# Optimization experiments

Measured on AMD Instinct MI355X. Metric: run time of the kernel, lower is better.

The kernel has to match this reference:

```python
import jax, jax.numpy as jnp
import numpy as np

B, T, F_IN, H = 512, 512, 64, 128
BN_EPS = 1e-3  # Keras BatchNormalization default epsilon


def setup_inputs() -> dict:
    key = jax.random.key(0)
    ks = jax.random.split(key, 12)
    x = jax.random.normal(ks[0], (B, T, F_IN), dtype=jnp.float32)
    # last channel is a discrete phase index in {0,1,2}, stored as float
    state = jax.random.randint(ks[1], (B, T, 1), 0, 3).astype(jnp.float32)
    inputs = jnp.concatenate([x, state], axis=-1)  # [B, T, F_IN+1]
    s = 1.0 / np.sqrt(H)
    return {
        "inputs": inputs,
        "Wx": jax.random.normal(ks[2], (F_IN, 3 * H), dtype=jnp.float32) * s,
        "Wh": jax.random.normal(ks[3], (H, 3 * H), dtype=jnp.float32) * s,
        "b": jax.random.normal(ks[4], (2, 3 * H), dtype=jnp.float32) * 0.01,
        "W_state": jax.random.normal(ks[5], (3, H), dtype=jnp.float32),
        "w1": jax.random.normal(ks[6], (H, 64), dtype=jnp.float32) * s,
        "b1": jnp.zeros((64,), jnp.float32),
        "gamma": jnp.ones((64,), jnp.float32),
        "beta": jnp.zeros((64,), jnp.float32),
        "mean": jnp.zeros((64,), jnp.float32),
        "var": jnp.ones((64,), jnp.float32),
        "w2": jax.random.normal(ks[7], (64, 1), dtype=jnp.float32) * 0.125,
        "b2": jnp.zeros((1,), jnp.float32),
    }


def _gru_final_state(x, Wx, Wh, b):
    # Keras GRU, reset_after=True (default): separate input / recurrent biases.
    b_in, b_rec = b[0], b[1]
    xw = x @ Wx + b_in                      # [B, T, 3H] (precompute input matmuls)
    xw_t = jnp.swapaxes(xw, 0, 1)           # [T, B, 3H]
    h0 = jnp.zeros((x.shape[0], Wh.shape[0]), x.dtype)

    def step(h, xw_step):
        rec = h @ Wh + b_rec                # [B, 3H]
        xz, xr, xh = jnp.split(xw_step, 3, axis=-1)
        rz, rr, rh = jnp.split(rec, 3, axis=-1)
        z = jax.nn.sigmoid(xz + rz)
        r = jax.nn.sigmoid(xr + rr)
        hh = jnp.tanh(xh + r * rh)
        h_new = z * h + (1.0 - z) * hh
        return h_new, None

    h_final, _ = jax.lax.scan(step, h0, xw_t)
    return h_final                          # [B, H]


def reference(inputs, Wx, Wh, b, W_state, w1, b1, gamma, beta, mean, var, w2, b2):
    x = inputs[:, :, :-1]                   # [B, T, F_IN]
    state = inputs[:, :, -1]                # [B, T]
    hidden = _gru_final_state(x, Wx, Wh, b)  # [B, H]
    idx = jnp.clip(state[:, -1].astype(jnp.int32), 0, W_state.shape[0] - 1)
    hidden = hidden + W_state[idx]          # gather-add phase effect
    h = jax.nn.relu(hidden @ w1 + b1)       # dense1
    # dropout: identity in inference mode
    h = (h - mean) * jax.lax.rsqrt(var + BN_EPS) * gamma + beta  # batchnorm (inference)
    return h @ w2 + b2                      # [B, 1]
```

## Files before the change

kernel.cpp:

```cpp
#include <hip/hip_runtime.h>
#include <hip/hip_bf16.h>

#define T_SEQ   512
#define H_DIM   128
#define N3H     384
#define HSW     128
#define XS      72

typedef float f32x4 __attribute__((ext_vector_type(4)));
typedef float f32x2 __attribute__((ext_vector_type(2)));
typedef float f32x4u __attribute__((ext_vector_type(4), aligned(4)));
typedef __bf16 bf16x8 __attribute__((ext_vector_type(8)));
typedef unsigned short us8 __attribute__((ext_vector_type(8)));
typedef unsigned short us4 __attribute__((ext_vector_type(4)));

static __device__ __forceinline__ unsigned short f2bf(float f) {
    unsigned int u = __builtin_bit_cast(unsigned int, f);
    u += 0x7FFFu + ((u >> 16) & 1u);
    return (unsigned short)(u >> 16);
}

static __device__ __forceinline__ void lds_barrier() {
    asm volatile("" ::: "memory");
    __builtin_amdgcn_s_waitcnt(0xC07F);
    __builtin_amdgcn_s_barrier();
    asm volatile("" ::: "memory");
}

static __device__ __forceinline__ bf16x8 ld8(const unsigned short* p) {
    return __builtin_bit_cast(bf16x8, *(const us8*)p);
}

__global__ __launch_bounds__(512, 1) void gru_fused(
    const float* __restrict__ inputs, const float* __restrict__ Wx,
    const float* __restrict__ Wh, const float* __restrict__ bias,
    const float* __restrict__ W_state, const float* __restrict__ w1,
    const float* __restrict__ b1, const float* __restrict__ gamma,
    const float* __restrict__ beta, const float* __restrict__ mean,
    const float* __restrict__ var, const float* __restrict__ w2,
    const float* __restrict__ b2, float* __restrict__ out)
{
    __shared__ __attribute__((aligned(16))) unsigned short hb[2][16 * HSW];
    __shared__ __attribute__((aligned(16))) unsigned short xb[2][16 * XS];
    __shared__ float hf[16][H_DIM + 1];

    const int tid  = threadIdx.x;
    const int w    = tid >> 6;
    const int lane = tid & 63;
    const int m    = lane & 15;
    const int q    = lane >> 4;
    const int b0   = blockIdx.x * 16;

    const float SCL0 = -1.4426950408889634f;
    const float SCL2 =  2.8853900817779268f;

    bf16x8 whB[3][4];
    bf16x8 wxB[3][2];
    float brec[3], bin[3];
#pragma unroll
    for (int g = 0; g < 3; ++g) {
        const float s = (g < 2) ? SCL0 : SCL2;
        const int col = (8 * g + w) * 16 + m;
#pragma unroll
        for (int k = 0; k < 4; ++k) {
            us8 tmp;
#pragma unroll
            for (int j = 0; j < 8; ++j) tmp[j] = f2bf(s * Wh[(32 * k + 8 * q + j) * N3H + col]);
            whB[g][k] = __builtin_bit_cast(bf16x8, tmp);
        }
#pragma unroll
        for (int k = 0; k < 2; ++k) {
            us8 tmp;
#pragma unroll
            for (int j = 0; j < 8; ++j) tmp[j] = f2bf(s * Wx[(32 * k + 8 * q + j) * N3H + col]);
            wxB[g][k] = __builtin_bit_cast(bf16x8, tmp);
        }
        bin[g]  = s * bias[col];
        brec[g] = s * bias[N3H + col];
    }

    int hro[4], hwo[4], xro[2];
#pragma unroll
    for (int k = 0; k < 4; ++k) hro[k] = m * HSW + (((4 * k + q) ^ (m & 7)) * 8);
#pragma unroll
    for (int i = 0; i < 4; ++i) {
        const int row = 4 * q + i;
        hwo[i] = row * HSW + (((2 * w + (m >> 3)) ^ (row & 7)) * 8) + (m & 7);
    }
#pragma unroll
    for (int k = 0; k < 2; ++k) xro[k] = m * XS + 32 * k + 8 * q;

    const int sr = tid >> 4, sc = tid & 15;
    const int xwoff = sr * XS + sc * 4;
    const float* xsrc = inputs + ((size_t)(b0 + sr) * T_SEQ) * 65 + sc * 4;

    auto xpack = [&](f32x4u v) -> us4 {
        us4 r; r[0] = f2bf(v[0]); r[1] = f2bf(v[1]); r[2] = f2bf(v[2]); r[3] = f2bf(v[3]);
        return r;
    };

    {
        unsigned int* p = (unsigned int*)hb[0];
        for (int i = tid; i < 16 * HSW / 2; i += 512) p[i] = 0;
    }
    if (tid < 256) {
        f32x4u v0 = *(const f32x4u*)(xsrc + 0 * 65);
        f32x4u v1 = *(const f32x4u*)(xsrc + 1 * 65);
        *(us4*)&xb[0][xwoff] = xpack(v0);
        *(us4*)&xb[1][xwoff] = xpack(v1);
    }
    lds_barrier();

    f32x4 xwA[3], xwB[3];
    {
        bf16x8 xa[2];
#pragma unroll
        for (int k = 0; k < 2; ++k) xa[k] = ld8(&xb[0][xro[k]]);
#pragma unroll
        for (int g = 0; g < 3; ++g) {
            f32x4 acc = { bin[g], bin[g], bin[g], bin[g] };
            acc = __builtin_amdgcn_mfma_f32_16x16x32_bf16(xa[0], wxB[g][0], acc, 0, 0, 0);
            acc = __builtin_amdgcn_mfma_f32_16x16x32_bf16(xa[1], wxB[g][1], acc, 0, 0, 0);
            xwA[g] = acc;
        }
    }

    f32x4u pf0 = {}, pf1 = {};
    if (tid < 256) pf0 = *(const f32x4u*)(xsrc + 2 * 65);

    f32x4 hreg = { 0.f, 0.f, 0.f, 0.f };

    auto step = [&](int t, f32x4* xw_cur, f32x4* xw_next,
                    f32x4u& pfLoad, f32x4u& pfUse,
                    const unsigned short* hcur, unsigned short* hnxt,
                    const unsigned short* xnxt, unsigned short* xwr) {
        if (tid < 256 && t <= T_SEQ - 4) pfLoad = *(const f32x4u*)(xsrc + (t + 3) * 65);

        lds_barrier();

        bf16x8 ha[4];
#pragma unroll
        for (int k = 0; k < 4; ++k) ha[k] = ld8(&hcur[hro[k]]);
        bf16x8 xa[2];
        if (t < T_SEQ - 1) {
#pragma unroll
            for (int k = 0; k < 2; ++k) xa[k] = ld8(&xnxt[xro[k]]);
        }

        f32x4 racc[3];
#pragma unroll
        for (int g = 0; g < 3; ++g) {
            f32x4 a1 = { brec[g], brec[g], brec[g], brec[g] };
            a1 = __builtin_amdgcn_mfma_f32_16x16x32_bf16(ha[0], whB[g][0], a1, 0, 0, 0);
            a1 = __builtin_amdgcn_mfma_f32_16x16x32_bf16(ha[1], whB[g][1], a1, 0, 0, 0);
            f32x4 a2 = { 0.f, 0.f, 0.f, 0.f };
            a2 = __builtin_amdgcn_mfma_f32_16x16x32_bf16(ha[2], whB[g][2], a2, 0, 0, 0);
            a2 = __builtin_amdgcn_mfma_f32_16x16x32_bf16(ha[3], whB[g][3], a2, 0, 0, 0);
            racc[g] = a1 + a2;
        }

        f32x4 hnew;
#pragma unroll
        for (int i = 0; i < 4; ++i) {
            const float ea = __builtin_amdgcn_exp2f(xw_cur[0][i] + racc[0][i]);
            const float eb = __builtin_amdgcn_exp2f(xw_cur[1][i] + racc[1][i]);
            const float Pa = 1.0f + ea, Pb = 1.0f + eb;
            const float D  = __builtin_amdgcn_rcpf(Pa * Pb);
            const float z  = Pb * D;
            const float r  = Pa * D;
            const float u  = fmaf(r, racc[2][i], xw_cur[2][i]);
            const float ec = __builtin_amdgcn_exp2f(u);
            const float hh = fmaf(-2.0f, __builtin_amdgcn_rcpf(1.0f + ec), 1.0f);
            hnew[i] = fmaf(z, hreg[i] - hh, hh);
        }
        hreg = hnew;

        if (t < T_SEQ - 1) {
#pragma unroll
            for (int g = 0; g < 3; ++g) {
                f32x4 acc = { bin[g], bin[g], bin[g], bin[g] };
                acc = __builtin_amdgcn_mfma_f32_16x16x32_bf16(xa[0], wxB[g][0], acc, 0, 0, 0);
                acc = __builtin_amdgcn_mfma_f32_16x16x32_bf16(xa[1], wxB[g][1], acc, 0, 0, 0);
                xw_next[g] = acc;
            }
        }

#pragma unroll
        for (int i = 0; i < 4; ++i) hnxt[hwo[i]] = f2bf(hnew[i]);

        if (tid < 256 && t <= T_SEQ - 3) *(us4*)&xwr[xwoff] = xpack(pfUse);
    };

    for (int t = 0; t < T_SEQ; t += 2) {
        step(t,     xwA, xwB, pf1, pf0, hb[0], hb[1], xb[1], xb[0]);
        step(t + 1, xwB, xwA, pf0, pf1, hb[1], hb[0], xb[0], xb[1]);
    }

#pragma unroll
    for (int i = 0; i < 4; ++i)
        hf[4 * q + i][16 * w + m] = hreg[i];
    __syncthreads();

    {
        const int row = tid >> 5;
        const int c0  = (tid & 31) * 4;
        const float sf = inputs[((size_t)(b0 + row) * T_SEQ + (T_SEQ - 1)) * 65 + 64];
        int si = (int)sf;
        si = si < 0 ? 0 : (si > 2 ? 2 : si);
#pragma unroll
        for (int c = 0; c < 4; ++c)
            hf[row][c0 + c] += W_state[si * H_DIM + c0 + c];
    }
    __syncthreads();

    {
        const int row = tid >> 5;
        const int jj  = (tid & 31) * 2;
        f32x2 acc = { b1[jj], b1[jj + 1] };
        for (int k = 0; k < H_DIM; ++k) {
            const float hv = hf[row][k];
            const f32x2 wv = *(const f32x2*)(w1 + k * 64 + jj);
            acc[0] = fmaf(hv, wv[0], acc[0]);
            acc[1] = fmaf(hv, wv[1], acc[1]);
        }
        float v = 0.0f;
#pragma unroll
        for (int ii = 0; ii < 2; ++ii) {
            const int j = jj + ii;
            float a = fmaxf(acc[ii], 0.0f);
            a = (a - mean[j]) * rsqrtf(var[j] + 1e-3f) * gamma[j] + beta[j];
            v = fmaf(a, w2[j], v);
        }
        v += __shfl_down(v, 16);
        v += __shfl_down(v, 8);
        v += __shfl_down(v, 4);
        v += __shfl_down(v, 2);
        v += __shfl_down(v, 1);
        if ((tid & 31) == 0) out[b0 + row] = v + b2[0];
    }
}

extern "C" void kernel_launch(void* const* d_in, const int* in_sizes, int n_in,
                              void* d_out, int out_size, void* d_ws, size_t ws_size,
                              hipStream_t stream) {
    (void)in_sizes; (void)n_in; (void)out_size; (void)d_ws; (void)ws_size;
    const float* inputs  = (const float*)d_in[0];
    const float* Wx      = (const float*)d_in[1];
    const float* Wh      = (const float*)d_in[2];
    const float* bias    = (const float*)d_in[3];
    const float* W_state = (const float*)d_in[4];
    const float* w1      = (const float*)d_in[5];
    const float* b1      = (const float*)d_in[6];
    const float* gamma   = (const float*)d_in[7];
    const float* beta    = (const float*)d_in[8];
    const float* mean    = (const float*)d_in[9];
    const float* var     = (const float*)d_in[10];
    const float* w2      = (const float*)d_in[11];
    const float* b2      = (const float*)d_in[12];
    float* out = (float*)d_out;

    gru_fused<<<32, 512, 0, stream>>>(inputs, Wx, Wh, bias, W_state, w1, b1,
                                      gamma, beta, mean, var, w2, b2, out);
}
```

Before: 476.6 us.

## Halve block to four waves, each wave computing two column groups

Cuts the block from 8 waves to 4, so each wave holds weights for two hidden-column groups and computes both gate sets per step. The second group's gate math is interleaved with the next step's input-projection MFMAs. Bf16 packing now uses the hardware v_cvt_pk_bf16_f32 instruction, and the epilogue is remapped for 256 threads. The goal is cheaper per-step barriers and better MFMA/VALU overlap on the serial recurrence. The cost is doubled per-wave work and register pressure, and only 32 blocks run on the device.

```diff
diff --git a/kernel.cpp b/kernel.cpp
--- a/kernel.cpp
+++ b/kernel.cpp
@@ -8,16 +8,21 @@
 #define XS      72
 
 typedef float f32x4 __attribute__((ext_vector_type(4)));
-typedef float f32x2 __attribute__((ext_vector_type(2)));
 typedef float f32x4u __attribute__((ext_vector_type(4), aligned(4)));
 typedef __bf16 bf16x8 __attribute__((ext_vector_type(8)));
 typedef unsigned short us8 __attribute__((ext_vector_type(8)));
-typedef unsigned short us4 __attribute__((ext_vector_type(4)));
+typedef unsigned int u32x2 __attribute__((ext_vector_type(2)));
 
 static __device__ __forceinline__ unsigned short f2bf(float f) {
     unsigned int u = __builtin_bit_cast(unsigned int, f);
     u += 0x7FFFu + ((u >> 16) & 1u);
     return (unsigned short)(u >> 16);
+}
+
+static __device__ __forceinline__ unsigned cvt_pk_bf16(float a, float b) {
+    unsigned r;
+    asm("v_cvt_pk_bf16_f32 %0, %1, %2" : "=v"(r) : "v"(a), "v"(b));
+    return r;
 }
 
 static __device__ __forceinline__ void lds_barrier() {
@@ -31,7 +36,7 @@
     return __builtin_bit_cast(bf16x8, *(const us8*)p);
 }
 
-__global__ __launch_bounds__(512, 1) void gru_fused(
+__global__ __launch_bounds__(256, 1) void gru_fused(
     const float* __restrict__ inputs, const float* __restrict__ Wx,
     const float* __restrict__ Wh, const float* __restrict__ bias,
     const float* __restrict__ W_state, const float* __restrict__ w1,
@@ -54,38 +59,48 @@
     const float SCL0 = -1.4426950408889634f;
     const float SCL2 =  2.8853900817779268f;
 
-    bf16x8 whB[3][4];
-    bf16x8 wxB[3][2];
-    float brec[3], bin[3];
-#pragma unroll
-    for (int g = 0; g < 3; ++g) {
-        const float s = (g < 2) ? SCL0 : SCL2;
-        const int col = (8 * g + w) * 16 + m;
-#pragma unroll
-        for (int k = 0; k < 4; ++k) {
-            us8 tmp;
-#pragma unroll
-            for (int j = 0; j < 8; ++j) tmp[j] = f2bf(s * Wh[(32 * k + 8 * q + j) * N3H + col]);
-            whB[g][k] = __builtin_bit_cast(bf16x8, tmp);
-        }
-#pragma unroll
-        for (int k = 0; k < 2; ++k) {
-            us8 tmp;
-#pragma unroll
-            for (int j = 0; j < 8; ++j) tmp[j] = f2bf(s * Wx[(32 * k + 8 * q + j) * N3H + col]);
-            wxB[g][k] = __builtin_bit_cast(bf16x8, tmp);
-        }
-        bin[g]  = s * bias[col];
-        brec[g] = s * bias[N3H + col];
-    }
-
-    int hro[4], hwo[4], xro[2];
+    bf16x8 whB[2][3][4];
+    bf16x8 wxB[2][3][2];
+    f32x4 binv[2][3], brecv[2][3];
+#pragma unroll
+    for (int c = 0; c < 2; ++c) {
+        const int cg = w + 4 * c;
+#pragma unroll
+        for (int g = 0; g < 3; ++g) {
+            const float s = (g < 2) ? SCL0 : SCL2;
+            const int col = (8 * g + cg) * 16 + m;
+#pragma unroll
+            for (int k = 0; k < 4; ++k) {
+                us8 tmp;
+#pragma unroll
+                for (int j = 0; j < 8; ++j) tmp[j] = f2bf(s * Wh[(32 * k + 8 * q + j) * N3H + col]);
+                whB[c][g][k] = __builtin_bit_cast(bf16x8, tmp);
+            }
+#pragma unroll
+            for (int k = 0; k < 2; ++k) {
+                us8 tmp;
+#pragma unroll
+                for (int j = 0; j < 8; ++j) tmp[j] = f2bf(s * Wx[(32 * k + 8 * q + j) * N3H + col]);
+                wxB[c][g][k] = __builtin_bit_cast(bf16x8, tmp);
+            }
+            const float bi = s * bias[col];
+            const float br = s * bias[N3H + col];
+            binv[c][g]  = (f32x4){ bi, bi, bi, bi };
+            brecv[c][g] = (f32x4){ br, br, br, br };
+        }
+    }
+
+    int hro[4], hwo[2][4], xro[2];
 #pragma unroll
     for (int k = 0; k < 4; ++k) hro[k] = m * HSW + (((4 * k + q) ^ (m & 7)) * 8);
 #pragma unroll
-    for (int i = 0; i < 4; ++i) {
-        const int row = 4 * q + i;
-        hwo[i] = row * HSW + (((2 * w + (m >> 3)) ^ (row & 7)) * 8) + (m & 7);
+    for (int c = 0; c < 2; ++c) {
+        const int cg = w + 4 * c;
+#pragma unroll
+        for (int i = 0; i < 4; ++i) {
+            const int row = 4 * q + i;
+            hwo[c][i] = row * HSW + (((2 * cg + (m >> 3)) ^ (row & 7)) * 8) + (m & 7);
+        }
     }
 #pragma unroll
     for (int k = 0; k < 2; ++k) xro[k] = m * XS + 32 * k + 8 * q;
@@ -94,47 +109,51 @@
     const int xwoff = sr * XS + sc * 4;
     const float* xsrc = inputs + ((size_t)(b0 + sr) * T_SEQ) * 65 + sc * 4;
 
-    auto xpack = [&](f32x4u v) -> us4 {
-        us4 r; r[0] = f2bf(v[0]); r[1] = f2bf(v[1]); r[2] = f2bf(v[2]); r[3] = f2bf(v[3]);
+    auto xpack = [&](f32x4u v) -> u32x2 {
+        u32x2 r;
+        r[0] = cvt_pk_bf16(v[0], v[1]);
+        r[1] = cvt_pk_bf16(v[2], v[3]);
         return r;
     };
 
     {
         unsigned int* p = (unsigned int*)hb[0];
-        for (int i = tid; i < 16 * HSW / 2; i += 512) p[i] = 0;
-    }
-    if (tid < 256) {
+        for (int i = tid; i < 16 * HSW / 2; i += 256) p[i] = 0;
+    }
+    {
         f32x4u v0 = *(const f32x4u*)(xsrc + 0 * 65);
         f32x4u v1 = *(const f32x4u*)(xsrc + 1 * 65);
-        *(us4*)&xb[0][xwoff] = xpack(v0);
-        *(us4*)&xb[1][xwoff] = xpack(v1);
+        *(u32x2*)&xb[0][xwoff] = xpack(v0);
+        *(u32x2*)&xb[1][xwoff] = xpack(v1);
     }
     lds_barrier();
 
-    f32x4 xwA[3], xwB[3];
+    f32x4 xwA[2][3], xwB[2][3];
     {
         bf16x8 xa[2];
 #pragma unroll
         for (int k = 0; k < 2; ++k) xa[k] = ld8(&xb[0][xro[k]]);
 #pragma unroll
-        for (int g = 0; g < 3; ++g) {
-            f32x4 acc = { bin[g], bin[g], bin[g], bin[g] };
-            acc = __builtin_amdgcn_mfma_f32_16x16x32_bf16(xa[0], wxB[g][0], acc, 0, 0, 0);
-            acc = __builtin_amdgcn_mfma_f32_16x16x32_bf16(xa[1], wxB[g][1], acc, 0, 0, 0);
-            xwA[g] = acc;
-        }
-    }
-
-    f32x4u pf0 = {}, pf1 = {};
-    if (tid < 256) pf0 = *(const f32x4u*)(xsrc + 2 * 65);
-
-    f32x4 hreg = { 0.f, 0.f, 0.f, 0.f };
-
-    auto step = [&](int t, f32x4* xw_cur, f32x4* xw_next,
+        for (int c = 0; c < 2; ++c)
+#pragma unroll
+            for (int g = 0; g < 3; ++g) {
+                f32x4 acc = binv[c][g];
+                acc = __builtin_amdgcn_mfma_f32_16x16x32_bf16(xa[0], wxB[c][g][0], acc, 0, 0, 0);
+                acc = __builtin_amdgcn_mfma_f32_16x16x32_bf16(xa[1], wxB[c][g][1], acc, 0, 0, 0);
+                xwA[c][g] = acc;
+            }
+    }
+
+    f32x4u pf0 = *(const f32x4u*)(xsrc + 2 * 65);
+    f32x4u pf1 = {};
+
+    f32x4 hreg[2] = { { 0.f, 0.f, 0.f, 0.f }, { 0.f, 0.f, 0.f, 0.f } };
+
+    auto step = [&](int t, f32x4 (*xw_cur)[3], f32x4 (*xw_next)[3],
                     f32x4u& pfLoad, f32x4u& pfUse,
                     const unsigned short* hcur, unsigned short* hnxt,
                     const unsigned short* xnxt, unsigned short* xwr) {
-        if (tid < 256 && t <= T_SEQ - 4) pfLoad = *(const f32x4u*)(xsrc + (t + 3) * 65);
+        if (t <= T_SEQ - 4) pfLoad = *(const f32x4u*)(xsrc + (t + 3) * 65);
 
         lds_barrier();
 
@@ -147,48 +166,62 @@
             for (int k = 0; k < 2; ++k) xa[k] = ld8(&xnxt[xro[k]]);
         }
 
-        f32x4 racc[3];
-#pragma unroll
-        for (int g = 0; g < 3; ++g) {
-            f32x4 a1 = { brec[g], brec[g], brec[g], brec[g] };
-            a1 = __builtin_amdgcn_mfma_f32_16x16x32_bf16(ha[0], whB[g][0], a1, 0, 0, 0);
-            a1 = __builtin_amdgcn_mfma_f32_16x16x32_bf16(ha[1], whB[g][1], a1, 0, 0, 0);
-            f32x4 a2 = { 0.f, 0.f, 0.f, 0.f };
-            a2 = __builtin_amdgcn_mfma_f32_16x16x32_bf16(ha[2], whB[g][2], a2, 0, 0, 0);
-            a2 = __builtin_amdgcn_mfma_f32_16x16x32_bf16(ha[3], whB[g][3], a2, 0, 0, 0);
-            racc[g] = a1 + a2;
-        }
-
-        f32x4 hnew;
-#pragma unroll
-        for (int i = 0; i < 4; ++i) {
-            const float ea = __builtin_amdgcn_exp2f(xw_cur[0][i] + racc[0][i]);
-            const float eb = __builtin_amdgcn_exp2f(xw_cur[1][i] + racc[1][i]);
-            const float Pa = 1.0f + ea, Pb = 1.0f + eb;
-            const float D  = __builtin_amdgcn_rcpf(Pa * Pb);
-            const float z  = Pb * D;
-            const float r  = Pa * D;
-            const float u  = fmaf(r, racc[2][i], xw_cur[2][i]);
-            const float ec = __builtin_amdgcn_exp2f(u);
-            const float hh = fmaf(-2.0f, __builtin_amdgcn_rcpf(1.0f + ec), 1.0f);
-            hnew[i] = fmaf(z, hreg[i] - hh, hh);
-        }
-        hreg = hnew;
+        f32x4 racc[2][3];
+#pragma unroll
+        for (int c = 0; c < 2; ++c)
+#pragma unroll
+            for (int g = 0; g < 3; ++g) {
+                f32x4 a1 = brecv[c][g];
+                a1 = __builtin_amdgcn_mfma_f32_16x16x32_bf16(ha[0], whB[c][g][0], a1, 0, 0, 0);
+                a1 = __builtin_amdgcn_mfma_f32_16x16x32_bf16(ha[1], whB[c][g][1], a1, 0, 0, 0);
+                f32x4 a2 = { 0.f, 0.f, 0.f, 0.f };
+                a2 = __builtin_amdgcn_mfma_f32_16x16x32_bf16(ha[2], whB[c][g][2], a2, 0, 0, 0);
+                a2 = __builtin_amdgcn_mfma_f32_16x16x32_bf16(ha[3], whB[c][g][3], a2, 0, 0, 0);
+                racc[c][g] = a1 + a2;
+            }
+
+        auto do_gates = [&](int c) {
+            f32x4 hnew;
+#pragma unroll
+            for (int i = 0; i < 4; ++i) {
+                const float ea = __builtin_amdgcn_exp2f(xw_cur[c][0][i] + racc[c][0][i]);
+                const float eb = __builtin_amdgcn_exp2f(xw_cur[c][1][i] + racc[c][1][i]);
+                const float Pa = 1.0f + ea, Pb = 1.0f + eb;
+                const float D  = __builtin_amdgcn_rcpf(Pa * Pb);
+                const float z  = Pb * D;
+                const float r  = Pa * D;
+                const float u  = fmaf(r, racc[c][2][i], xw_cur[c][2][i]);
+                const float ec = __builtin_amdgcn_exp2f(u);
+                const float hh = fmaf(-2.0f, __builtin_amdgcn_rcpf(1.0f + ec), 1.0f);
+                hnew[i] = fmaf(z, hreg[c][i] - hh, hh);
+            }
+            hreg[c] = hnew;
+            const float h0 = hnew[0], h1 = hnew[1], h2 = hnew[2], h3 = hnew[3];
+            const unsigned p01 = cvt_pk_bf16(h0, h1);
+            const unsigned p23 = cvt_pk_bf16(h2, h3);
+            hnxt[hwo[c][0]] = (unsigned short)(p01);
+            hnxt[hwo[c][1]] = (unsigned short)(p01 >> 16);
+            hnxt[hwo[c][2]] = (unsigned short)(p23);
+            hnxt[hwo[c][3]] = (unsigned short)(p23 >> 16);
+        };
+
+        do_gates(0);
 
         if (t < T_SEQ - 1) {
 #pragma unroll
-            for (int g = 0; g < 3; ++g) {
-                f32x4 acc = { bin[g], bin[g], bin[g], bin[g] };
-                acc = __builtin_amdgcn_mfma_f32_16x16x32_bf16(xa[0], wxB[g][0], acc, 0, 0, 0);
-                acc = __builtin_amdgcn_mfma_f32_16x16x32_bf16(xa[1], wxB[g][1], acc, 0, 0, 0);
-                xw_next[g] = acc;
-            }
-        }
-
-#pragma unroll
-        for (int i = 0; i < 4; ++i) hnxt[hwo[i]] = f2bf(hnew[i]);
-
-        if (tid < 256 && t <= T_SEQ - 3) *(us4*)&xwr[xwoff] = xpack(pfUse);
+            for (int c = 0; c < 2; ++c)
+#pragma unroll
+                for (int g = 0; g < 3; ++g) {
+                    f32x4 acc = binv[c][g];
+                    acc = __builtin_amdgcn_mfma_f32_16x16x32_bf16(xa[0], wxB[c][g][0], acc, 0, 0, 0);
+                    acc = __builtin_amdgcn_mfma_f32_16x16x32_bf16(xa[1], wxB[c][g][1], acc, 0, 0, 0);
+                    xw_next[c][g] = acc;
+                }
+        }
+
+        do_gates(1);
+
+        if (t <= T_SEQ - 3) *(u32x2*)&xwr[xwoff] = xpack(pfUse);
     };
 
     for (int t = 0; t < T_SEQ; t += 2) {
@@ -197,46 +230,47 @@
     }
 
 #pragma unroll
-    for (int i = 0; i < 4; ++i)
-        hf[4 * q + i][16 * w + m] = hreg[i];
+    for (int c = 0; c < 2; ++c)
+#pragma unroll
+        for (int i = 0; i < 4; ++i)
+            hf[4 * q + i][(w + 4 * c) * 16 + m] = hreg[c][i];
     __syncthreads();
 
     {
-        const int row = tid >> 5;
-        const int c0  = (tid & 31) * 4;
+        const int row = tid >> 4;
+        const int c0  = (tid & 15) * 8;
         const float sf = inputs[((size_t)(b0 + row) * T_SEQ + (T_SEQ - 1)) * 65 + 64];
         int si = (int)sf;
         si = si < 0 ? 0 : (si > 2 ? 2 : si);
 #pragma unroll
-        for (int c = 0; c < 4; ++c)
+        for (int c = 0; c < 8; ++c)
             hf[row][c0 + c] += W_state[si * H_DIM + c0 + c];
     }
     __syncthreads();
 
     {
-        const int row = tid >> 5;
-        const int jj  = (tid & 31) * 2;
-        f32x2 acc = { b1[jj], b1[jj + 1] };
+        const int row = tid >> 4;
+        const int j0  = (tid & 15) * 4;
+        f32x4 acc = { b1[j0], b1[j0 + 1], b1[j0 + 2], b1[j0 + 3] };
         for (int k = 0; k < H_DIM; ++k) {
             const float hv = hf[row][k];
-            const f32x2 wv = *(const f32x2*)(w1 + k * 64 + jj);
-            acc[0] = fmaf(hv, wv[0], acc[0]);
-            acc[1] = fmaf(hv, wv[1], acc[1]);
+            const f32x4u wv = *(const f32x4u*)(w1 + k * 64 + j0);
+#pragma unroll
+            for (int c = 0; c < 4; ++c) acc[c] = fmaf(hv, wv[c], acc[c]);
         }
         float v = 0.0f;
 #pragma unroll
-        for (int ii = 0; ii < 2; ++ii) {
-            const int j = jj + ii;
-            float a = fmaxf(acc[ii], 0.0f);
+        for (int c = 0; c < 4; ++c) {
+            const int j = j0 + c;
+            float a = fmaxf(acc[c], 0.0f);
             a = (a - mean[j]) * rsqrtf(var[j] + 1e-3f) * gamma[j] + beta[j];
             v = fmaf(a, w2[j], v);
         }
-        v += __shfl_down(v, 16);
         v += __shfl_down(v, 8);
         v += __shfl_down(v, 4);
         v += __shfl_down(v, 2);
         v += __shfl_down(v, 1);
-        if ((tid & 31) == 0) out[b0 + row] = v + b2[0];
+        if ((tid & 15) == 0) out[b0 + row] = v + b2[0];
     }
 }
 
@@ -259,6 +293,6 @@
     const float* b2      = (const float*)d_in[12];
     float* out = (float*)d_out;
 
-    gru_fused<<<32, 512, 0, stream>>>(inputs, Wx, Wh, bias, W_state, w1, b1,
+    gru_fused<<<32, 256, 0, stream>>>(inputs, Wx, Wh, bias, W_state, w1, b1,
                                       gamma, beta, mean, var, w2, b2, out);
 }
```

Measured after the change: 531.4 us. 1.11x slower.
